# Kernel tuning notes

Hardware: AMD Instinct MI355X
Metric: run time of the kernel (lower is better)

## Reference

```python
import jax, jax.numpy as jnp
import numpy as np


def setup_inputs() -> dict:
    key = jax.random.key(0)
    k1, k2, k3, k4 = jax.random.split(key, 4)
    B, D_IN, D, N, A = 32, 2048, 128, 400000, 7
    return {
        "x": jax.random.normal(k1, (B, D_IN), dtype=jnp.float32),
        "W_enc": jax.random.normal(k2, (D_IN, D), dtype=jnp.float32) * 0.02,
        "b_enc": jnp.zeros((D,), dtype=jnp.float32),
        "reps": jax.random.normal(k3, (N, D), dtype=jnp.float32),
        "actions": jax.random.normal(k4, (N, A), dtype=jnp.float32),
        "k": 5,
    }


def reference(x, W_enc, b_enc, reps, actions, k):
    # encoder embed: [B, D]
    batch_rep = x @ W_enc + b_enc
    # euclidean cdist: [B, N]
    sq = (
        jnp.sum(batch_rep * batch_rep, axis=-1, keepdims=True)
        + jnp.sum(reps * reps, axis=-1)[None, :]
        - 2.0 * (batch_rep @ reps.T)
    )
    dists = jnp.sqrt(jnp.maximum(sq, 1e-12))
    # top-k smallest distances
    neg_topk, indices = jax.lax.top_k(-dists, k)  # [B, k]
    top_k_distances = -neg_topk
    # gather actions: [B, k, A]
    top_k_actions = actions[indices]
    # softmax(-distance) weights: [B, k]
    weights = jax.nn.softmax(-top_k_distances, axis=1)
    # weighted average: [B, A]
    pred = jnp.sum(top_k_actions * weights[..., None], axis=1)
    return pred
```

## Files before the change

### kernel.cpp

```cpp
#include <hip/hip_runtime.h>
#include <math.h>

#define BATCH 32
#define DIN   2048
#define DK    128
#define NREPS 400000
#define ACT   7
#define NGRP  (NREPS / 64)

__device__ __forceinline__ void topk_insert(float s, int n,
    float& d0, float& d1, float& d2, float& d3, float& d4,
    int& i0, int& i1, int& i2, int& i3, int& i4)
{
    if (s < d4) {
        if (s < d3) {
            d4 = d3; i4 = i3;
            if (s < d2) {
                d3 = d2; i3 = i2;
                if (s < d1) {
                    d2 = d1; i2 = i1;
                    if (s < d0) { d1 = d0; i1 = i0; d0 = s; i0 = n; }
                    else        { d1 = s;  i1 = n; }
                } else { d2 = s; i2 = n; }
            } else { d3 = s; i3 = n; }
        } else { d4 = s; i4 = n; }
    }
}

__global__ __launch_bounds__(256) void encoder_kernel(
    const float* __restrict__ x, const float* __restrict__ W,
    const float* __restrict__ be, float* __restrict__ brept,
    float* __restrict__ brnorm)
{
    __shared__ float xs[DIN];
    __shared__ float part[256];
    __shared__ float vrow[DK];
    const int b = blockIdx.x, t = threadIdx.x;

    const float4* x4 = (const float4*)(x + (size_t)b * DIN);
    float4* xs4 = (float4*)xs;
    xs4[t]       = x4[t];
    xs4[t + 256] = x4[t + 256];
    __syncthreads();

    const int d = t & 127, h = t >> 7;
    const float* Wp = W + (size_t)(h * 1024) * DK + d;
    const float* xp = xs + h * 1024;
    float a0 = 0.f, a1 = 0.f, a2 = 0.f, a3 = 0.f;
    for (int i = 0; i < 1024; i += 4) {
        a0 = fmaf(xp[i],     Wp[(size_t)i * DK],       a0);
        a1 = fmaf(xp[i + 1], Wp[(size_t)(i + 1) * DK], a1);
        a2 = fmaf(xp[i + 2], Wp[(size_t)(i + 2) * DK], a2);
        a3 = fmaf(xp[i + 3], Wp[(size_t)(i + 3) * DK], a3);
    }
    part[t] = (a0 + a1) + (a2 + a3);
    __syncthreads();
    if (t < DK) {
        float v = part[t] + part[t + 128] + be[t];
        brept[t * BATCH + b] = -2.0f * v;
        vrow[t] = v * v;
    }
    __syncthreads();
    if (t == 0) {
        float s = 0.f;
        for (int i = 0; i < DK; i++) s += vrow[i];
        brnorm[b] = s;
    }
}

__global__ __launch_bounds__(256, 4) void dist_topk_kernel(
    const float* __restrict__ reps, const float* __restrict__ brt,
    float* __restrict__ pd, int* __restrict__ pi, int nwaves)
{
    __shared__ float wdist[4 * 64 * 36];
    const int t = threadIdx.x, g = blockIdx.x;
    const int wid = t >> 6, ln = t & 63;
    const int b = ln & 31, h = ln >> 5;
    float* wd = wdist + wid * (64 * 36);

    float d0 = 3.0e38f, d1 = 3.0e38f, d2 = 3.0e38f, d3 = 3.0e38f, d4 = 3.0e38f;
    int   i0 = 0, i1 = 0, i2 = 0, i3 = 0, i4 = 0;

    for (int grp = g * 4 + wid; grp < NGRP; grp += nwaves) {
        const float4* rp = (const float4*)(reps + (size_t)(grp * 64 + ln) * DK);
        float acc[32];
        #pragma unroll
        for (int i = 0; i < 32; i++) acc[i] = 0.f;
        float nrm = 0.f;

        #pragma unroll 1
        for (int c = 0; c < 4; c++) {
            float4 r[8];
            #pragma unroll
            for (int q = 0; q < 8; q++) r[q] = rp[c * 8 + q];
            const float* bp0 = brt + c * 32 * BATCH;
            #pragma unroll
            for (int q = 0; q < 8; q++) {
                const float4 rr = r[q];
                nrm = fmaf(rr.x, rr.x, nrm);
                nrm = fmaf(rr.y, rr.y, nrm);
                nrm = fmaf(rr.z, rr.z, nrm);
                nrm = fmaf(rr.w, rr.w, nrm);
                const float* bp = bp0 + q * 4 * BATCH;
                #pragma unroll
                for (int bb = 0; bb < 32; bb++) {
                    float a = acc[bb];
                    a = fmaf(bp[bb],             rr.x, a);
                    a = fmaf(bp[BATCH + bb],     rr.y, a);
                    a = fmaf(bp[2 * BATCH + bb], rr.z, a);
                    a = fmaf(bp[3 * BATCH + bb], rr.w, a);
                    acc[bb] = a;
                }
            }
        }

        #pragma unroll
        for (int q = 0; q < 8; q++) {
            float4 v;
            v.x = acc[4 * q]     + nrm;
            v.y = acc[4 * q + 1] + nrm;
            v.z = acc[4 * q + 2] + nrm;
            v.w = acc[4 * q + 3] + nrm;
            *(float4*)&wd[ln * 36 + 4 * q] = v;
        }
        asm volatile("s_waitcnt lgkmcnt(0)" ::: "memory");

        const int nb = grp * 64;
        #pragma unroll 4
        for (int s = 0; s < 32; s++) {
            const int row = h * 32 + s;
            const float dv = wd[row * 36 + b];
            topk_insert(dv, nb + row, d0, d1, d2, d3, d4, i0, i1, i2, i3, i4);
        }
        asm volatile("s_waitcnt lgkmcnt(0)" ::: "memory");
    }

    __syncthreads();
    float* cD = wdist;
    int*   cI = (int*)(wdist + 1280);
    {
        const int base = t * 5;
        cD[base]     = d0; cI[base]     = i0;
        cD[base + 1] = d1; cI[base + 1] = i1;
        cD[base + 2] = d2; cI[base + 2] = i2;
        cD[base + 3] = d3; cI[base + 3] = i3;
        cD[base + 4] = d4; cI[base + 4] = i4;
    }
    __syncthreads();
    if (t < 32) {
        float e0 = 3.0e38f, e1 = 3.0e38f, e2 = 3.0e38f, e3 = 3.0e38f, e4 = 3.0e38f;
        int   j0 = 0, j1 = 0, j2 = 0, j3 = 0, j4 = 0;
        for (int j = 0; j < 8; j++) {
            const int base = (t + 32 * j) * 5;
            #pragma unroll
            for (int e = 0; e < 5; e++)
                topk_insert(cD[base + e], cI[base + e],
                            e0, e1, e2, e3, e4, j0, j1, j2, j3, j4);
        }
        const int ob = (g * BATCH + t) * 5;
        pd[ob] = e0; pd[ob + 1] = e1; pd[ob + 2] = e2; pd[ob + 3] = e3; pd[ob + 4] = e4;
        pi[ob] = j0; pi[ob + 1] = j1; pi[ob + 2] = j2; pi[ob + 3] = j3; pi[ob + 4] = j4;
    }
}

__global__ __launch_bounds__(256) void final_kernel(
    const float* __restrict__ pd, const int* __restrict__ pi,
    const float* __restrict__ brnorm, const float* __restrict__ actions,
    float* __restrict__ out, int G)
{
    __shared__ float lD[256 * 5];
    __shared__ int   lI[256 * 5];
    __shared__ float sD[32 * 5];
    __shared__ int   sI[32 * 5];
    const int b = blockIdx.x, t = threadIdx.x;

    float d0 = 3.0e38f, d1 = 3.0e38f, d2 = 3.0e38f, d3 = 3.0e38f, d4 = 3.0e38f;
    int   i0 = 0, i1 = 0, i2 = 0, i3 = 0, i4 = 0;
    for (int g = t; g < G; g += 256) {
        const int base = (g * BATCH + b) * 5;
        #pragma unroll
        for (int e = 0; e < 5; e++)
            topk_insert(pd[base + e], pi[base + e],
                        d0, d1, d2, d3, d4, i0, i1, i2, i3, i4);
    }
    lD[t * 5] = d0; lD[t * 5 + 1] = d1; lD[t * 5 + 2] = d2; lD[t * 5 + 3] = d3; lD[t * 5 + 4] = d4;
    lI[t * 5] = i0; lI[t * 5 + 1] = i1; lI[t * 5 + 2] = i2; lI[t * 5 + 3] = i3; lI[t * 5 + 4] = i4;
    __syncthreads();
    if (t < 32) {
        d0 = d1 = d2 = d3 = d4 = 3.0e38f; i0 = i1 = i2 = i3 = i4 = 0;
        for (int s = 0; s < 8; s++) {
            const int base = (t * 8 + s) * 5;
            #pragma unroll
            for (int e = 0; e < 5; e++)
                topk_insert(lD[base + e], lI[base + e],
                            d0, d1, d2, d3, d4, i0, i1, i2, i3, i4);
        }
        sD[t * 5] = d0; sD[t * 5 + 1] = d1; sD[t * 5 + 2] = d2; sD[t * 5 + 3] = d3; sD[t * 5 + 4] = d4;
        sI[t * 5] = i0; sI[t * 5 + 1] = i1; sI[t * 5 + 2] = i2; sI[t * 5 + 3] = i3; sI[t * 5 + 4] = i4;
    }
    __syncthreads();
    if (t == 0) {
        d0 = d1 = d2 = d3 = d4 = 3.0e38f; i0 = i1 = i2 = i3 = i4 = 0;
        for (int s = 0; s < 32; s++) {
            const int base = s * 5;
            #pragma unroll
            for (int e = 0; e < 5; e++)
                topk_insert(sD[base + e], sI[base + e],
                            d0, d1, d2, d3, d4, i0, i1, i2, i3, i4);
        }
        const float bn = brnorm[b];
        float dist[5]; int idx[5];
        dist[0] = d0; dist[1] = d1; dist[2] = d2; dist[3] = d3; dist[4] = d4;
        idx[0] = i0; idx[1] = i1; idx[2] = i2; idx[3] = i3; idx[4] = i4;
        float dmin = 3.0e38f;
        #pragma unroll
        for (int e = 0; e < 5; e++) {
            dist[e] = sqrtf(fmaxf(dist[e] + bn, 1e-12f));
            dmin = fminf(dmin, dist[e]);
        }
        float w[5], wsum = 0.f;
        #pragma unroll
        for (int e = 0; e < 5; e++) { w[e] = expf(dmin - dist[e]); wsum += w[e]; }
        const float inv = 1.0f / wsum;
        for (int a = 0; a < ACT; a++) {
            float o = 0.f;
            #pragma unroll
            for (int e = 0; e < 5; e++)
                o = fmaf(w[e], actions[(size_t)idx[e] * ACT + a], o);
            out[b * ACT + a] = o * inv;
        }
    }
}

extern "C" void kernel_launch(void* const* d_in, const int* in_sizes, int n_in,
                              void* d_out, int out_size, void* d_ws, size_t ws_size,
                              hipStream_t stream)
{
    (void)in_sizes; (void)n_in; (void)out_size;
    const float* x       = (const float*)d_in[0];
    const float* W       = (const float*)d_in[1];
    const float* be      = (const float*)d_in[2];
    const float* reps    = (const float*)d_in[3];
    const float* actions = (const float*)d_in[4];

    float* ws     = (float*)d_ws;
    float* brept  = ws;
    float* brnorm = ws + 4096;
    float* pd     = ws + 4224;

    int G = 782;
    {
        const size_t avail_f = ws_size / 4;
        if (avail_f < 4224 + (size_t)G * 320) {
            long fit = ((long)avail_f - 4224) / 320;
            G = (fit < 1) ? 1 : (int)fit;
            if (G > 782) G = 782;
        }
    }
    int* pi = (int*)(pd + (size_t)G * BATCH * 5);
    const int nwaves = G * 4;

    encoder_kernel  <<<32, 256, 0, stream>>>(x, W, be, brept, brnorm);
    dist_topk_kernel<<<G,  256, 0, stream>>>(reps, brept, pd, pi, nwaves);
    final_kernel    <<<32, 256, 0, stream>>>(pd, pi, brnorm, actions, (float*)d_out, G);
}
```

Before: 495.0 us.

## Compute distances with split-bf16 MFMA and rerank top-10 in exact fp32

Replaces the scalar FP32 FMA distance loop with bf16 MFMA instructions. Operands are split into high and low bf16 parts and three products are summed to approximate fp32 accuracy. Rep tiles are staged through LDS with register prefetch of the next tile, and the grid size and occupancy bound change. The final kernel keeps the top-10 candidates and recomputes their distances exactly in fp32 before picking the top-5, guarding against ranking errors from the approximate products. The cost is extra LDS traffic and added conversion work in exchange for matrix-core throughput.

```diff
diff --git a/kernel.cpp b/kernel.cpp
--- a/kernel.cpp
+++ b/kernel.cpp
@@ -6,7 +6,17 @@
 #define DK    128
 #define NREPS 400000
 #define ACT   7
-#define NGRP  (NREPS / 64)
+#define TROWS 64
+#define NTILE (NREPS / TROWS)
+#define STRIDE 132
+#define GDEF  694
+
+typedef __attribute__((ext_vector_type(8))) __bf16 bf16x8;
+typedef __attribute__((ext_vector_type(4))) float  f32x4;
+
+static __device__ __forceinline__ __bf16 bits2bf(unsigned short v) {
+    union { unsigned short u; __bf16 b; } x; x.u = v; return x.b;
+}
 
 __device__ __forceinline__ void topk_insert(float s, int n,
     float& d0, float& d1, float& d2, float& d3, float& d4,
@@ -68,110 +78,169 @@
     }
 }
 
-__global__ __launch_bounds__(256, 4) void dist_topk_kernel(
+__global__ __launch_bounds__(256, 2) void dist_topk_kernel(
     const float* __restrict__ reps, const float* __restrict__ brt,
-    float* __restrict__ pd, int* __restrict__ pi, int nwaves)
-{
-    __shared__ float wdist[4 * 64 * 36];
-    const int t = threadIdx.x, g = blockIdx.x;
-    const int wid = t >> 6, ln = t & 63;
-    const int b = ln & 31, h = ln >> 5;
-    float* wd = wdist + wid * (64 * 36);
-
-    float d0 = 3.0e38f, d1 = 3.0e38f, d2 = 3.0e38f, d3 = 3.0e38f, d4 = 3.0e38f;
-    int   i0 = 0, i1 = 0, i2 = 0, i3 = 0, i4 = 0;
-
-    for (int grp = g * 4 + wid; grp < NGRP; grp += nwaves) {
-        const float4* rp = (const float4*)(reps + (size_t)(grp * 64 + ln) * DK);
-        float acc[32];
-        #pragma unroll
-        for (int i = 0; i < 32; i++) acc[i] = 0.f;
-        float nrm = 0.f;
-
-        #pragma unroll 1
-        for (int c = 0; c < 4; c++) {
-            float4 r[8];
-            #pragma unroll
-            for (int q = 0; q < 8; q++) r[q] = rp[c * 8 + q];
-            const float* bp0 = brt + c * 32 * BATCH;
-            #pragma unroll
-            for (int q = 0; q < 8; q++) {
-                const float4 rr = r[q];
-                nrm = fmaf(rr.x, rr.x, nrm);
-                nrm = fmaf(rr.y, rr.y, nrm);
-                nrm = fmaf(rr.z, rr.z, nrm);
-                nrm = fmaf(rr.w, rr.w, nrm);
-                const float* bp = bp0 + q * 4 * BATCH;
-                #pragma unroll
-                for (int bb = 0; bb < 32; bb++) {
-                    float a = acc[bb];
-                    a = fmaf(bp[bb],             rr.x, a);
-                    a = fmaf(bp[BATCH + bb],     rr.y, a);
-                    a = fmaf(bp[2 * BATCH + bb], rr.z, a);
-                    a = fmaf(bp[3 * BATCH + bb], rr.w, a);
-                    acc[bb] = a;
-                }
-            }
-        }
-
-        #pragma unroll
-        for (int q = 0; q < 8; q++) {
-            float4 v;
-            v.x = acc[4 * q]     + nrm;
-            v.y = acc[4 * q + 1] + nrm;
-            v.z = acc[4 * q + 2] + nrm;
-            v.w = acc[4 * q + 3] + nrm;
-            *(float4*)&wd[ln * 36 + 4 * q] = v;
-        }
-        asm volatile("s_waitcnt lgkmcnt(0)" ::: "memory");
-
-        const int nb = grp * 64;
-        #pragma unroll 4
-        for (int s = 0; s < 32; s++) {
-            const int row = h * 32 + s;
-            const float dv = wd[row * 36 + b];
-            topk_insert(dv, nb + row, d0, d1, d2, d3, d4, i0, i1, i2, i3, i4);
-        }
-        asm volatile("s_waitcnt lgkmcnt(0)" ::: "memory");
-    }
-
-    __syncthreads();
-    float* cD = wdist;
-    int*   cI = (int*)(wdist + 1280);
+    float* __restrict__ pd, int* __restrict__ pi)
+{
+    __shared__ float tile[TROWS * STRIDE];
+    __shared__ float nrmb[TROWS];
+    const int t = threadIdx.x, g = blockIdx.x, G = gridDim.x;
+    const int wv = t >> 6, ln = t & 63;
+    const int c = ln & 15, quad = ln >> 4;
+    const int srow = t >> 2, sq = t & 3;
+
+    bf16x8 Bh[2][4], Bl[2][4];
+    #pragma unroll
+    for (int nt = 0; nt < 2; nt++)
+        #pragma unroll
+        for (int ks = 0; ks < 4; ks++) {
+            bf16x8 h, l;
+            #pragma unroll
+            for (int j = 0; j < 8; j++) {
+                const float f = brt[(ks * 32 + quad * 8 + j) * BATCH + nt * 16 + c];
+                const unsigned u = __float_as_uint(f);
+                h[j] = bits2bf((unsigned short)(u >> 16));
+                const float lf = f - __uint_as_float(u & 0xFFFF0000u);
+                l[j] = bits2bf((unsigned short)(__float_as_uint(lf) >> 16));
+            }
+            Bh[nt][ks] = h; Bl[nt][ks] = l;
+        }
+
+    float tA0 = 3.0e38f, tA1 = 3.0e38f, tA2 = 3.0e38f, tA3 = 3.0e38f, tA4 = 3.0e38f;
+    int   jA0 = 0, jA1 = 0, jA2 = 0, jA3 = 0, jA4 = 0;
+    float tB0 = 3.0e38f, tB1 = 3.0e38f, tB2 = 3.0e38f, tB3 = 3.0e38f, tB4 = 3.0e38f;
+    int   jB0 = 0, jB1 = 0, jB2 = 0, jB3 = 0, jB4 = 0;
+
     {
-        const int base = t * 5;
-        cD[base]     = d0; cI[base]     = i0;
-        cD[base + 1] = d1; cI[base + 1] = i1;
-        cD[base + 2] = d2; cI[base + 2] = i2;
-        cD[base + 3] = d3; cI[base + 3] = i3;
-        cD[base + 4] = d4; cI[base + 4] = i4;
+        const float4* gs = (const float4*)reps + (size_t)g * 2048 + srow * 32 + sq;
+        float4 r[8];
+        #pragma unroll
+        for (int i = 0; i < 8; i++) r[i] = gs[4 * i];
+        float s = 0.f;
+        #pragma unroll
+        for (int i = 0; i < 8; i++) {
+            s = fmaf(r[i].x, r[i].x, s); s = fmaf(r[i].y, r[i].y, s);
+            s = fmaf(r[i].z, r[i].z, s); s = fmaf(r[i].w, r[i].w, s);
+        }
+        s += __shfl_xor(s, 1); s += __shfl_xor(s, 2);
+        #pragma unroll
+        for (int i = 0; i < 8; i++)
+            *(f32x4*)&tile[srow * STRIDE + (sq + 4 * i) * 4] =
+                (f32x4){r[i].x, r[i].y, r[i].z, r[i].w};
+        if ((t & 3) == 0) nrmb[srow] = s;
+    }
+    __syncthreads();
+
+    int it = g;
+    while (true) {
+        const int itn = it + G;
+        const bool have = itn < NTILE;
+        float4 r[8];
+        if (have) {
+            const float4* gs = (const float4*)reps + (size_t)itn * 2048 + srow * 32 + sq;
+            #pragma unroll
+            for (int i = 0; i < 8; i++) r[i] = gs[4 * i];
+        }
+
+        f32x4 C0 = {0.f, 0.f, 0.f, 0.f}, C1 = {0.f, 0.f, 0.f, 0.f};
+        #pragma unroll
+        for (int ks = 0; ks < 4; ks++) {
+            const float* ap = &tile[(wv * 16 + c) * STRIDE + ks * 32 + quad * 8];
+            const f32x4 a0 = *(const f32x4*)ap;
+            const f32x4 a1 = *(const f32x4*)(ap + 4);
+            bf16x8 ah, al;
+            #pragma unroll
+            for (int j = 0; j < 8; j++) {
+                const float f = (j < 4) ? a0[j] : a1[j - 4];
+                const unsigned u = __float_as_uint(f);
+                ah[j] = bits2bf((unsigned short)(u >> 16));
+                const float lf = f - __uint_as_float(u & 0xFFFF0000u);
+                al[j] = bits2bf((unsigned short)(__float_as_uint(lf) >> 16));
+            }
+            C0 = __builtin_amdgcn_mfma_f32_16x16x32_bf16(ah, Bh[0][ks], C0, 0, 0, 0);
+            C0 = __builtin_amdgcn_mfma_f32_16x16x32_bf16(ah, Bl[0][ks], C0, 0, 0, 0);
+            C0 = __builtin_amdgcn_mfma_f32_16x16x32_bf16(al, Bh[0][ks], C0, 0, 0, 0);
+            C1 = __builtin_amdgcn_mfma_f32_16x16x32_bf16(ah, Bh[1][ks], C1, 0, 0, 0);
+            C1 = __builtin_amdgcn_mfma_f32_16x16x32_bf16(ah, Bl[1][ks], C1, 0, 0, 0);
+            C1 = __builtin_amdgcn_mfma_f32_16x16x32_bf16(al, Bh[1][ks], C1, 0, 0, 0);
+        }
+        {
+            const int rowb = wv * 16 + quad * 4;
+            const int nb = it * TROWS + rowb;
+            #pragma unroll
+            for (int reg = 0; reg < 4; reg++) {
+                const float nr = nrmb[rowb + reg];
+                const float s0 = C0[reg] + nr;
+                const float s1 = C1[reg] + nr;
+                topk_insert(s0, nb + reg, tA0, tA1, tA2, tA3, tA4, jA0, jA1, jA2, jA3, jA4);
+                topk_insert(s1, nb + reg, tB0, tB1, tB2, tB3, tB4, jB0, jB1, jB2, jB3, jB4);
+            }
+        }
+        __syncthreads();
+        if (have) {
+            float s = 0.f;
+            #pragma unroll
+            for (int i = 0; i < 8; i++) {
+                s = fmaf(r[i].x, r[i].x, s); s = fmaf(r[i].y, r[i].y, s);
+                s = fmaf(r[i].z, r[i].z, s); s = fmaf(r[i].w, r[i].w, s);
+            }
+            s += __shfl_xor(s, 1); s += __shfl_xor(s, 2);
+            #pragma unroll
+            for (int i = 0; i < 8; i++)
+                *(f32x4*)&tile[srow * STRIDE + (sq + 4 * i) * 4] =
+                    (f32x4){r[i].x, r[i].y, r[i].z, r[i].w};
+            if ((t & 3) == 0) nrmb[srow] = s;
+        }
+        __syncthreads();
+        if (!have) break;
+        it = itn;
+    }
+
+    float* cD = tile;
+    int*   cI = (int*)(tile + 2560);
+    {
+        const int base0 = ((0 * 16 + c) * 16 + (wv * 4 + quad)) * 5;
+        cD[base0]     = tA0; cI[base0]     = jA0;
+        cD[base0 + 1] = tA1; cI[base0 + 1] = jA1;
+        cD[base0 + 2] = tA2; cI[base0 + 2] = jA2;
+        cD[base0 + 3] = tA3; cI[base0 + 3] = jA3;
+        cD[base0 + 4] = tA4; cI[base0 + 4] = jA4;
+        const int base1 = ((16 + c) * 16 + (wv * 4 + quad)) * 5;
+        cD[base1]     = tB0; cI[base1]     = jB0;
+        cD[base1 + 1] = tB1; cI[base1 + 1] = jB1;
+        cD[base1 + 2] = tB2; cI[base1 + 2] = jB2;
+        cD[base1 + 3] = tB3; cI[base1 + 3] = jB3;
+        cD[base1 + 4] = tB4; cI[base1 + 4] = jB4;
     }
     __syncthreads();
     if (t < 32) {
-        float e0 = 3.0e38f, e1 = 3.0e38f, e2 = 3.0e38f, e3 = 3.0e38f, e4 = 3.0e38f;
-        int   j0 = 0, j1 = 0, j2 = 0, j3 = 0, j4 = 0;
-        for (int j = 0; j < 8; j++) {
-            const int base = (t + 32 * j) * 5;
+        float d0 = 3.0e38f, d1 = 3.0e38f, d2 = 3.0e38f, d3 = 3.0e38f, d4 = 3.0e38f;
+        int   i0 = 0, i1 = 0, i2 = 0, i3 = 0, i4 = 0;
+        for (int s2 = 0; s2 < 16; s2++) {
+            const int base = (t * 16 + s2) * 5;
             #pragma unroll
             for (int e = 0; e < 5; e++)
                 topk_insert(cD[base + e], cI[base + e],
-                            e0, e1, e2, e3, e4, j0, j1, j2, j3, j4);
+                            d0, d1, d2, d3, d4, i0, i1, i2, i3, i4);
         }
         const int ob = (g * BATCH + t) * 5;
-        pd[ob] = e0; pd[ob + 1] = e1; pd[ob + 2] = e2; pd[ob + 3] = e3; pd[ob + 4] = e4;
-        pi[ob] = j0; pi[ob + 1] = j1; pi[ob + 2] = j2; pi[ob + 3] = j3; pi[ob + 4] = j4;
+        pd[ob] = d0; pd[ob + 1] = d1; pd[ob + 2] = d2; pd[ob + 3] = d3; pd[ob + 4] = d4;
+        pi[ob] = i0; pi[ob + 1] = i1; pi[ob + 2] = i2; pi[ob + 3] = i3; pi[ob + 4] = i4;
     }
 }
 
 __global__ __launch_bounds__(256) void final_kernel(
     const float* __restrict__ pd, const int* __restrict__ pi,
     const float* __restrict__ brnorm, const float* __restrict__ actions,
+    const float* __restrict__ reps, const float* __restrict__ brt,
     float* __restrict__ out, int G)
 {
     __shared__ float lD[256 * 5];
     __shared__ int   lI[256 * 5];
     __shared__ float sD[32 * 5];
     __shared__ int   sI[32 * 5];
+    __shared__ int   exi[10];
+    __shared__ float exq[10];
     const int b = blockIdx.x, t = threadIdx.x;
 
     float d0 = 3.0e38f, d1 = 3.0e38f, d2 = 3.0e38f, d3 = 3.0e38f, d4 = 3.0e38f;
@@ -200,33 +269,62 @@
     }
     __syncthreads();
     if (t == 0) {
-        d0 = d1 = d2 = d3 = d4 = 3.0e38f; i0 = i1 = i2 = i3 = i4 = 0;
-        for (int s = 0; s < 32; s++) {
-            const int base = s * 5;
-            #pragma unroll
-            for (int e = 0; e < 5; e++)
-                topk_insert(sD[base + e], sI[base + e],
-                            d0, d1, d2, d3, d4, i0, i1, i2, i3, i4);
-        }
+        float dd[10]; int ii[10];
+        #pragma unroll
+        for (int j = 0; j < 10; j++) { dd[j] = 3.0e38f; ii[j] = 0; }
+        for (int s2 = 0; s2 < 160; s2++) {
+            const float v = sD[s2]; const int ix = sI[s2];
+            if (v < dd[9]) {
+                int j = 9;
+                while (j > 0 && dd[j - 1] > v) { dd[j] = dd[j - 1]; ii[j] = ii[j - 1]; j--; }
+                dd[j] = v; ii[j] = ix;
+            }
+        }
+        #pragma unroll
+        for (int j = 0; j < 10; j++) exi[j] = ii[j];
+    }
+    __syncthreads();
+    if (t < 80) {
+        const int cand = t >> 3, seg = t & 7;
+        const int row = exi[cand];
+        const float4* rp = (const float4*)(reps + (size_t)row * DK) + seg * 4;
+        float s = 0.f;
+        #pragma unroll
+        for (int q = 0; q < 4; q++) {
+            const float4 v = rp[q];
+            const int k0 = seg * 16 + q * 4;
+            s += v.x * v.x + brt[(k0 + 0) * BATCH + b] * v.x;
+            s += v.y * v.y + brt[(k0 + 1) * BATCH + b] * v.y;
+            s += v.z * v.z + brt[(k0 + 2) * BATCH + b] * v.z;
+            s += v.w * v.w + brt[(k0 + 3) * BATCH + b] * v.w;
+        }
+        s += __shfl_xor(s, 1); s += __shfl_xor(s, 2); s += __shfl_xor(s, 4);
+        if ((t & 7) == 0) exq[cand] = s;
+    }
+    __syncthreads();
+    if (t == 0) {
         const float bn = brnorm[b];
-        float dist[5]; int idx[5];
-        dist[0] = d0; dist[1] = d1; dist[2] = d2; dist[3] = d3; dist[4] = d4;
-        idx[0] = i0; idx[1] = i1; idx[2] = i2; idx[3] = i3; idx[4] = i4;
-        float dmin = 3.0e38f;
-        #pragma unroll
+        float dd[10];
+        #pragma unroll
+        for (int j = 0; j < 10; j++) dd[j] = sqrtf(fmaxf(exq[j] + bn, 1e-12f));
+        float dist5[5]; int idx5[5];
+        bool used[10] = {false,false,false,false,false,false,false,false,false,false};
         for (int e = 0; e < 5; e++) {
-            dist[e] = sqrtf(fmaxf(dist[e] + bn, 1e-12f));
-            dmin = fminf(dmin, dist[e]);
-        }
+            int am = -1; float mv = 3.0e38f;
+            for (int j = 0; j < 10; j++)
+                if (!used[j] && dd[j] < mv) { mv = dd[j]; am = j; }
+            used[am] = true; dist5[e] = mv; idx5[e] = exi[am];
+        }
+        const float dmin = dist5[0];
         float w[5], wsum = 0.f;
         #pragma unroll
-        for (int e = 0; e < 5; e++) { w[e] = expf(dmin - dist[e]); wsum += w[e]; }
+        for (int e = 0; e < 5; e++) { w[e] = expf(dmin - dist5[e]); wsum += w[e]; }
         const float inv = 1.0f / wsum;
         for (int a = 0; a < ACT; a++) {
             float o = 0.f;
             #pragma unroll
             for (int e = 0; e < 5; e++)
-                o = fmaf(w[e], actions[(size_t)idx[e] * ACT + a], o);
+                o = fmaf(w[e], actions[(size_t)idx5[e] * ACT + a], o);
             out[b * ACT + a] = o * inv;
         }
     }
@@ -248,19 +346,19 @@
     float* brnorm = ws + 4096;
     float* pd     = ws + 4224;
 
-    int G = 782;
+    int G = GDEF;
     {
         const size_t avail_f = ws_size / 4;
         if (avail_f < 4224 + (size_t)G * 320) {
             long fit = ((long)avail_f - 4224) / 320;
             G = (fit < 1) ? 1 : (int)fit;
-            if (G > 782) G = 782;
+            if (G > GDEF) G = GDEF;
         }
     }
     int* pi = (int*)(pd + (size_t)G * BATCH * 5);
-    const int nwaves = G * 4;
 
     encoder_kernel  <<<32, 256, 0, stream>>>(x, W, be, brept, brnorm);
-    dist_topk_kernel<<<G,  256, 0, stream>>>(reps, brept, pd, pi, nwaves);
-    final_kernel    <<<32, 256, 0, stream>>>(pd, pi, brnorm, actions, (float*)d_out, G);
-}
+    dist_topk_kernel<<<G,  256, 0, stream>>>(reps, brept, pd, pi);
+    final_kernel    <<<32, 256, 0, stream>>>(pd, pi, brnorm, actions, reps, brept,
+                                             (float*)d_out, G);
+}
```

New measurement: 496.1 us. Within noise of the previous version (+0.2%).
